# Kernel optimization log

Hardware: AMD Instinct MI355X
Metric: run time of the kernel (lower is better)

## Reference

```python
import jax, jax.numpy as jnp
import numpy as np

B, SEQ_IN, N, IN_DIM = 8, 12, 1000, 2
HID, HEADS = 128, 8
DH = HID // HEADS
E = 16000
INTERVAL, SCALE = 4, 1.0
LRELU_SLOPE = 0.2


def _layer_norm(x):
    # LayerNorm over last dim, elementwise_affine=False, eps=1e-5
    mu = jnp.mean(x, axis=-1, keepdims=True)
    var = jnp.mean((x - mu) ** 2, axis=-1, keepdims=True)
    return (x - mu) / jnp.sqrt(var + 1e-5)


def _edge_softmax(e, dst, n):
    # e: [E, HEADS]; softmax over edges sharing the same destination node
    m = jax.ops.segment_max(e, dst, num_segments=n)
    ex = jnp.exp(e - m[dst])
    s = jax.ops.segment_sum(ex, dst, num_segments=n)
    return ex / (s[dst] + 1e-16)


def _gat(x, src, dst, w_gat, a_l, a_r):
    # x: [B, N, HID] -> [B, N, HID]; single-layer multi-head GATConv
    b, n, _ = x.shape
    h = (x @ w_gat).reshape(b, n, HEADS, DH)
    el = jnp.einsum('bnhd,hd->bnh', h, a_l)
    er = jnp.einsum('bnhd,hd->bnh', h, a_r)
    e = jax.nn.leaky_relu(el[:, src] + er[:, dst], LRELU_SLOPE)  # [B, E, HEADS]
    alpha = jax.vmap(_edge_softmax, in_axes=(0, None, None))(e, dst, n)
    msg = h[:, src] * alpha[..., None]  # [B, E, HEADS, DH]
    agg = jax.vmap(lambda m: jax.ops.segment_sum(m, dst, num_segments=n))(msg)
    return agg.reshape(b, n, HID)


def _odeint_rk4(f, y0, t):
    # fixed-step RK4 over the time grid t (stand-in for torchdiffeq.odeint)
    def step(y, ts):
        t0, t1 = ts
        dt = t1 - t0
        k1 = f(y)
        k2 = f(y + 0.5 * dt * k1)
        k3 = f(y + 0.5 * dt * k2)
        k4 = f(y + dt * k3)
        return y + (dt / 6.0) * (k1 + 2.0 * k2 + 2.0 * k3 + k4), None
    y, _ = jax.lax.scan(jax.checkpoint(step), y0, (t[:-1], t[1:]))
    return y


def setup_inputs() -> dict:
    key = jax.random.key(0)
    ks = jax.random.split(key, 12)
    s = 0.05
    inputs = jax.random.normal(ks[0], (B, SEQ_IN, N, IN_DIM), dtype=jnp.float32)
    src = jax.random.randint(ks[1], (E,), 0, N, dtype=jnp.int32)
    dst = jax.random.randint(ks[2], (E,), 0, N, dtype=jnp.int32)
    w_in = jax.random.normal(ks[3], (IN_DIM, HID), jnp.float32) * s
    b_in = jnp.zeros((HID,), jnp.float32)
    w_gat = jax.random.normal(ks[4], (HID, HID), jnp.float32) * s
    a_l = jax.random.normal(ks[5], (HEADS, DH), jnp.float32) * s
    a_r = jax.random.normal(ks[6], (HEADS, DH), jnp.float32) * s
    w_W = jax.random.normal(ks[7], (HID, HID), jnp.float32) * s
    b_W = jnp.zeros((HID,), jnp.float32)
    w_U = jax.random.normal(ks[8], (HID, HID), jnp.float32) * s
    b_U = jnp.zeros((HID,), jnp.float32)
    w_o1 = jax.random.normal(ks[9], (HID, HID), jnp.float32) * s
    b_o1 = jnp.zeros((HID,), jnp.float32)
    w_o2 = jax.random.normal(ks[10], (HID, HID), jnp.float32) * s
    b_o2 = jnp.zeros((HID,), jnp.float32)
    return {"inputs": inputs, "src": src, "dst": dst, "w_in": w_in, "b_in": b_in,
            "w_gat": w_gat, "a_l": a_l, "a_r": a_r, "w_W": w_W, "b_W": b_W,
            "w_U": w_U, "b_U": b_U, "w_o1": w_o1, "b_o1": b_o1, "w_o2": w_o2, "b_o2": b_o2}


def reference(inputs, src, dst, w_in, b_in, w_gat, a_l, a_r, w_W, b_W,
              w_U, b_U, w_o1, b_o1, w_o2, b_o2):
    h = inputs @ w_in + b_in  # [B, SEQ_IN, N, HID]
    t = jnp.linspace(0.0, 1.0, INTERVAL + 1, dtype=jnp.float32) * SCALE
    f = lambda y: _gat(y, src, dst, w_gat, a_l, a_r)
    ret = h[:, 0]  # y0 = first timestep
    for idx in range(SEQ_IN):
        ret = _odeint_rk4(f, ret, t)  # take final time point
        if idx != 0:
            ret = jnp.tanh(ret @ w_W + b_W + h[:, idx] @ w_U + b_U)
        ret = _layer_norm(ret)
    out = ret[:, None]  # [B, 1, N, HID]  (view + unsqueeze + transpose)
    out = jnp.tanh(out @ w_o1 + b_o1) @ w_o2 + b_o2
    return out
```

## Files before the change

### kernel.cpp

```cpp
#include <hip/hip_runtime.h>

#define NNODE 1000
#define NBATCH 8
#define SEQL 12
#define NHEAD 8
#define DHEAD 16
#define HID 128
#define NEDGE 16000
#define NROWS (NBATCH*NNODE)
#define RPB 32
#define NBLK_P 256
#define NBLK_B 32
#define BARSTRIDE 64
#define PTHREADS 1024
#define ORPB 16
#define NBLK_O (NROWS/ORPB)
#define DT 0.25f
#define ECAP 768
#define SPIN_LIMIT 2000000ULL
#define WSTRIDE 136
#define WLO (128*WSTRIDE)
#define HSTR 144

#define OFF_MASK  32
#define OFF_GMASK 48
#define OFF_GCNT  56
#define HWREG_XCC_ID 6164


typedef unsigned short u16;
typedef unsigned int   u32;
typedef unsigned long long u64;
typedef __attribute__((ext_vector_type(8))) short bf16x8;
typedef __attribute__((ext_vector_type(4))) float f32x4;
typedef __attribute__((ext_vector_type(4))) unsigned int u32x4;

__device__ __forceinline__ u16 f2bf(float f){
  u32 x = __float_as_uint(f);
  return (u16)((x + 0x7fffu + ((x>>16)&1u)) >> 16);
}
__device__ __forceinline__ float bf2f(u16 u){ return __uint_as_float(((u32)u)<<16); }

__device__ __forceinline__ u64 ld_agent_u64(const u16* p){
  return __hip_atomic_load(reinterpret_cast<const u64*>(p),
                           __ATOMIC_RELAXED, __HIP_MEMORY_SCOPE_AGENT);
}
__device__ __forceinline__ void st_agent_u64(u16* p, u64 v){
  __hip_atomic_store(reinterpret_cast<u64*>(p), v,
                     __ATOMIC_RELAXED, __HIP_MEMORY_SCOPE_AGENT);
}
__device__ __forceinline__ float ld_agent_f32(const float* p){
  u32 v = __hip_atomic_load(reinterpret_cast<const u32*>(p),
                            __ATOMIC_RELAXED, __HIP_MEMORY_SCOPE_AGENT);
  return __uint_as_float(v);
}
__device__ __forceinline__ void st_agent_f32(float* p, float v){
  __hip_atomic_store(reinterpret_cast<u32*>(p), __float_as_uint(v),
                     __ATOMIC_RELAXED, __HIP_MEMORY_SCOPE_AGENT);
}

__device__ __forceinline__ void inv_l1(){
  asm volatile("buffer_inv sc0\n\ts_waitcnt vmcnt(0)" ::: "memory");
}

__device__ __forceinline__ int poll_l2(int* p){
  int exp = -1;
  __hip_atomic_compare_exchange_strong(p, &exp, -1,
      __ATOMIC_RELAXED, __ATOMIC_RELAXED, __HIP_MEMORY_SCOPE_WORKGROUP);
  return exp;
}

__device__ __forceinline__ void grid_bar2(int* bar, int target, bool l2){
  __syncthreads();
  if (threadIdx.x == 0){
    unsigned long long t0;
    if (l2){
      __hip_atomic_fetch_add(bar, 1, __ATOMIC_RELAXED, __HIP_MEMORY_SCOPE_WORKGROUP);
      t0 = __builtin_amdgcn_s_memrealtime();
      while (poll_l2(bar) < target){
        __builtin_amdgcn_s_sleep(2);
        if (__builtin_amdgcn_s_memrealtime() - t0 > SPIN_LIMIT) break;
      }
    } else {
      __hip_atomic_fetch_add(bar, 1, __ATOMIC_RELEASE, __HIP_MEMORY_SCOPE_AGENT);
      t0 = __builtin_amdgcn_s_memrealtime();
      while (__hip_atomic_load(bar, __ATOMIC_RELAXED, __HIP_MEMORY_SCOPE_AGENT) < target){
        __builtin_amdgcn_s_sleep(2);
        if (__builtin_amdgcn_s_memrealtime() - t0 > SPIN_LIMIT) break;
      }
    }
  }
  __syncthreads();
}

__device__ __forceinline__ void startup_bar(int* cnt){
  __syncthreads();
  if (threadIdx.x == 0){
    __hip_atomic_fetch_add(cnt, 1, __ATOMIC_RELEASE, __HIP_MEMORY_SCOPE_AGENT);
    unsigned long long t0 = __builtin_amdgcn_s_memrealtime();
    while (__hip_atomic_load(cnt, __ATOMIC_RELAXED, __HIP_MEMORY_SCOPE_AGENT) < NBLK_P){
      __builtin_amdgcn_s_sleep(2);
      if (__builtin_amdgcn_s_memrealtime() - t0 > SPIN_LIMIT) break;
    }
  }
  __syncthreads();
}

template<int NT>
__device__ __forceinline__ void load_W(float* Wl, const float* g, int tid){
  #pragma unroll
  for (int c = 0; c < (HID*HID/4)/NT; ++c){
    int e = (c*NT + tid)*4;
    *reinterpret_cast<float4*>(Wl + e) = *reinterpret_cast<const float4*>(g + e);
  }
}

__device__ __forceinline__ void load_WT_split(u16* WbT, const float* g, int tid){
  #pragma unroll
  for (int c = 0; c < 16; ++c){
    int flat = c*PTHREADS + tid;
    int k = flat >> 7, n = flat & 127;
    float v = g[flat];
    u16 hi = f2bf(v);
    u16 lo = f2bf(v - bf2f(hi));
    WbT[n*WSTRIDE + k]       = hi;
    WbT[WLO + n*WSTRIDE + k] = lo;
  }
}

__device__ __forceinline__ void gemm128_1(const float* Wl, const float* yt, int fg, int rs,
                                          float o[4]){
  float a0[4]={0.f,0.f,0.f,0.f};
  #pragma unroll 4
  for (int k=0;k<HID;k+=4){
    float4 ya = *reinterpret_cast<const float4*>(yt + rs*HID + k);
    #pragma unroll
    for (int kk=0;kk<4;++kk){
      const float* wr = Wl + (k+kk)*HID + fg*4;
      float av = (&ya.x)[kk];
      #pragma unroll
      for (int i=0;i<4;++i) a0[i] = fmaf(wr[i], av, a0[i]);
    }
  }
  #pragma unroll
  for (int i=0;i<4;++i) o[i]=a0[i];
}

template<int RSTEP>
__device__ __forceinline__ void gemm128(const float* Wl, const float* yt, int fg, int rs,
                                        float o0[4], float o1[4]){
  float a0[4]={0.f,0.f,0.f,0.f}, a1[4]={0.f,0.f,0.f,0.f};
  #pragma unroll 4
  for (int k=0;k<HID;k+=4){
    float4 ya = *reinterpret_cast<const float4*>(yt + rs*HID + k);
    float4 yb = *reinterpret_cast<const float4*>(yt + (rs+RSTEP)*HID + k);
    #pragma unroll
    for (int kk=0;kk<4;++kk){
      const float* wr = Wl + (k+kk)*HID + fg*4;
      float av = (&ya.x)[kk];
      float bv = (&yb.x)[kk];
      #pragma unroll
      for (int i=0;i<4;++i){
        float w = wr[i];
        a0[i] = fmaf(w, av, a0[i]);
        a1[i] = fmaf(w, bv, a1[i]);
      }
    }
  }
  #pragma unroll
  for (int i=0;i<4;++i){ o0[i]=a0[i]; o1[i]=a1[i]; }
}

__device__ __forceinline__ void pack_y(u16* yt_bf, int rA, int off8, const float y[8]){
  uint4 w;
  w.x = (u32)f2bf(y[0]) | ((u32)f2bf(y[1])<<16);
  w.y = (u32)f2bf(y[2]) | ((u32)f2bf(y[3])<<16);
  w.z = (u32)f2bf(y[4]) | ((u32)f2bf(y[5])<<16);
  w.w = (u32)f2bf(y[6]) | ((u32)f2bf(y[7])<<16);
  *reinterpret_cast<uint4*>(yt_bf + rA*WSTRIDE + off8) = w;
}

__device__ __forceinline__ void edge_acc(const u32x4 q, float el, float erh,
                                         float acc[8], float& sum){
  float hv[8];
  hv[0]=__uint_as_float(q[0]<<16); hv[1]=__uint_as_float(q[0]&0xffff0000u);
  hv[2]=__uint_as_float(q[1]<<16); hv[3]=__uint_as_float(q[1]&0xffff0000u);
  hv[4]=__uint_as_float(q[2]<<16); hv[5]=__uint_as_float(q[2]&0xffff0000u);
  hv[6]=__uint_as_float(q[3]<<16); hv[7]=__uint_as_float(q[3]&0xffff0000u);
  const float x = el + erh;
  const float w = __expf(fminf(fmaxf(x, 0.2f*x), 30.f));
  sum += w;
  #pragma unroll
  for (int i=0;i<8;++i) acc[i] = fmaf(w, hv[i], acc[i]);
}

template<bool L2>
__device__ __forceinline__ void gather_f(const u16* __restrict__ h_rd,
    const int* __restrict__ eptr, int e_lo, int e_hi, int sbase, int off8, int hd,
    float erh, float acc[8], float& sum)
{
  if constexpr (L2){
    int e = e_lo;
    for (; e + 4 <= e_hi; e += 4){
      const u16* r0 = h_rd + (size_t)(sbase + eptr[e+0])*HSTR;
      const u16* r1 = h_rd + (size_t)(sbase + eptr[e+1])*HSTR;
      const u16* r2 = h_rd + (size_t)(sbase + eptr[e+2])*HSTR;
      const u16* r3 = h_rd + (size_t)(sbase + eptr[e+3])*HSTR;
      u32x4 q0 = *reinterpret_cast<const u32x4*>(r0 + off8);
      u32x4 q1 = *reinterpret_cast<const u32x4*>(r1 + off8);
      u32x4 q2 = *reinterpret_cast<const u32x4*>(r2 + off8);
      u32x4 q3 = *reinterpret_cast<const u32x4*>(r3 + off8);
      float x0 = reinterpret_cast<const float*>(r0 + 128)[hd];
      float x1 = reinterpret_cast<const float*>(r1 + 128)[hd];
      float x2 = reinterpret_cast<const float*>(r2 + 128)[hd];
      float x3 = reinterpret_cast<const float*>(r3 + 128)[hd];
      edge_acc(q0, x0, erh, acc, sum);
      edge_acc(q1, x1, erh, acc, sum);
      edge_acc(q2, x2, erh, acc, sum);
      edge_acc(q3, x3, erh, acc, sum);
    }
    for (; e < e_hi; ++e){
      const u16* r = h_rd + (size_t)(sbase + eptr[e])*HSTR;
      u32x4 q = *reinterpret_cast<const u32x4*>(r + off8);
      float x = reinterpret_cast<const float*>(r + 128)[hd];
      edge_acc(q, x, erh, acc, sum);
    }
  } else {
    for (int e = e_lo; e < e_hi; ++e){
      const u16* r = h_rd + (size_t)(sbase + eptr[e])*HSTR;
      const u64 L = ld_agent_u64(r + off8);
      const u64 H = ld_agent_u64(r + off8 + 4);
      const float x = ld_agent_f32(reinterpret_cast<const float*>(r + 128) + hd);
      u32x4 v;
      v[0]=(u32)L; v[1]=(u32)(L>>32); v[2]=(u32)H; v[3]=(u32)(H>>32);
      edge_acc(v, x, erh, acc, sum);
    }
  }
}

__device__ __forceinline__ void h_stage(const u16* yt_bf, u16* ht_bf, const u16* WbT,
    int mt, int nt, int quad, int lc,
    int fg, int rs, int rowF, bool actF, bool l2,
    u16* __restrict__ h_wr, float* er_l, const float ar4[4], const float al4[4])
{
  f32x4 c0 = {0.f,0.f,0.f,0.f}, c1 = {0.f,0.f,0.f,0.f};
  const u16* arow = yt_bf + (mt*16 + lc)*WSTRIDE;
  const u16* brow = WbT  + (nt*16 + lc)*WSTRIDE;
  #pragma unroll
  for (int k0 = 0; k0 < 4; ++k0){
    const int off = k0*32 + quad*8;
    bf16x8 a  = *reinterpret_cast<const bf16x8*>(arow + off);
    bf16x8 bh = *reinterpret_cast<const bf16x8*>(brow + off);
    bf16x8 bl = *reinterpret_cast<const bf16x8*>(brow + WLO + off);
    if (k0 & 1){
      c1 = __builtin_amdgcn_mfma_f32_16x16x32_bf16(a, bh, c1, 0, 0, 0);
      c1 = __builtin_amdgcn_mfma_f32_16x16x32_bf16(a, bl, c1, 0, 0, 0);
    } else {
      c0 = __builtin_amdgcn_mfma_f32_16x16x32_bf16(a, bh, c0, 0, 0, 0);
      c0 = __builtin_amdgcn_mfma_f32_16x16x32_bf16(a, bl, c0, 0, 0, 0);
    }
  }
  {
    const int col = nt*16 + lc;
    #pragma unroll
    for (int r = 0; r < 4; ++r)
      ht_bf[(mt*16 + quad*4 + r)*WSTRIDE + col] = f2bf(c0[r] + c1[r]);
  }
  __syncthreads();
  const u64 pk = *reinterpret_cast<const u64*>(ht_bf + rs*WSTRIDE + fg*4);
  if (actF){
    if (l2) *reinterpret_cast<u64*>(h_wr + (size_t)rowF*HSTR + fg*4) = pk;
    else    st_agent_u64(h_wr + (size_t)rowF*HSTR + fg*4, pk);
  }
  const float h0 = bf2f((u16)pk),       h1 = bf2f((u16)(pk>>16));
  const float h2 = bf2f((u16)(pk>>32)), h3 = bf2f((u16)(pk>>48));
  float er = 0.f, el = 0.f;
  er = fmaf(h0, ar4[0], er); er = fmaf(h1, ar4[1], er);
  er = fmaf(h2, ar4[2], er); er = fmaf(h3, ar4[3], er);
  el = fmaf(h0, al4[0], el); el = fmaf(h1, al4[1], el);
  el = fmaf(h2, al4[2], el); el = fmaf(h3, al4[3], el);
  er += __shfl_xor(er,1); er += __shfl_xor(er,2);
  el += __shfl_xor(el,1); el += __shfl_xor(el,2);
  if ((fg & 3) == 0 && actF){
    er_l[rs*NHEAD + (fg>>2)] = er;
    float* elp = reinterpret_cast<float*>(h_wr + (size_t)rowF*HSTR + 128);
    if (l2) elp[fg>>2] = el;
    else    st_agent_f32(elp + (fg>>2), el);
  }
}

__global__ void csr_kernel(const int* __restrict__ src, const int* __restrict__ dst,
                           int* __restrict__ row_start, int* __restrict__ edge_src,
                           int* __restrict__ bar){
  __shared__ int cnt[1024];
  __shared__ int scanb[1024];
  __shared__ int cur[1024];
  int tid = threadIdx.x;
  if (tid < NBATCH*BARSTRIDE) bar[tid] = 0;
  cnt[tid] = 0;
  __syncthreads();
  for (int e = tid; e < NEDGE; e += 1024) atomicAdd(&cnt[dst[e]], 1);
  __syncthreads();
  int v = cnt[tid];
  scanb[tid] = v;
  __syncthreads();
  for (int off=1; off<1024; off<<=1){
    int t = (tid >= off) ? scanb[tid-off] : 0;
    __syncthreads();
    scanb[tid] += t;
    __syncthreads();
  }
  int incl = scanb[tid];
  if (tid < NNODE){ cur[tid] = incl - v; row_start[tid+1] = incl; }
  if (tid == 0) row_start[0] = 0;
  __syncthreads();
  for (int e = tid; e < NEDGE; e += 1024){
    int d = dst[e];
    int pos = atomicAdd(&cur[d], 1);
    edge_src[pos] = src[e];
  }
}

struct PArgs {
  u16* hb0; u16* hb1; float* y_out;
  const int* row_start; const int* edge_src;
  const float* w_gat; const float* a_l; const float* a_r;
  const float* inputs; const float* w_in; const float* b_in;
  const float* w_W; const float* b_W; const float* w_U; const float* b_U;
  int* bar;
};

__global__ void __launch_bounds__(PTHREADS, 4) persist(PArgs p)
{
  __shared__ __align__(16) u16 WbT[2*128*WSTRIDE];
  __shared__ __align__(16) u16 yt_bf[RPB*WSTRIDE];
  __shared__ __align__(16) u16 ht_bf[RPB*WSTRIDE];
  __shared__ float zt[RPB*HID];
  __shared__ int   esrc_l[ECAP];
  __shared__ int   eoff[RPB+1];
  __shared__ int   degs_s[RPB];
  __shared__ float er_l[RPB*NHEAD];
  __shared__ int   use_l2_s;
  float* const Wlf = reinterpret_cast<float*>(WbT);

  const int tid  = threadIdx.x;
  const int bat   = blockIdx.x & 7;
  const int slot  = blockIdx.x >> 3;
  const int row0  = bat * NNODE + slot * RPB;
  const int nrows = (slot == 31) ? (NNODE - 31*RPB) : RPB;
  int* const bar_b = p.bar + bat * BARSTRIDE;
  const int tA = tid & 15, seg = (tid >> 4) & 1, rA = tid >> 5;
  const bool actA = rA < nrows;
  const int nA     = slot*RPB + rA;
  const int nAs    = actA ? nA : 0;
  const int sbase  = bat * NNODE;
  const int hd   = tA >> 1;
  const int off8 = tA * 8;
  const int fg = tid & 31, rs = tid >> 5;
  const bool actF = rs < nrows;
  const int rowF = row0 + rs;
  const int hd2 = fg >> 2, db = (fg & 3) * 4;
  const int wv = tid >> 6, lane = tid & 63, quad = lane >> 4, lc = lane & 15;
  const int mt = wv & 1, nt = wv >> 1;

  int s0r = 0, degr = 0;
  if (actA){ s0r = p.row_start[nA]; degr = p.row_start[nA+1] - s0r; }
  if ((tid & 31) == 0) degs_s[rA] = degr;
  __syncthreads();
  if (tid == 0){
    int o = 0;
    #pragma unroll
    for (int r = 0; r < RPB; ++r){ eoff[r] = o; o += degs_s[r]; }
    eoff[RPB] = o;
  }
  __syncthreads();
  const int* eptr;
  if (eoff[RPB] <= ECAP){
    const int eb = eoff[rA];
    for (int e = tA + 16*seg; e < degr; e += 32) esrc_l[eb + e] = p.edge_src[s0r + e];
    eptr = esrc_l + eb;
  } else {
    eptr = p.edge_src + s0r;
  }

  float ar4[4], al4[4];
  #pragma unroll
  for (int i=0;i<4;++i){
    ar4[i] = p.a_r[hd2*DHEAD + db + i];
    al4[i] = p.a_l[hd2*DHEAD + db + i];
  }

  load_WT_split(WbT, p.w_gat, tid);

  float yb8[8], ya8[8];
  {
    const float x0 = p.inputs[((bat*SEQL + 0)*NNODE + nAs)*2 + 0];
    const float x1 = p.inputs[((bat*SEQL + 0)*NNODE + nAs)*2 + 1];
    #pragma unroll
    for (int i=0;i<8;++i){
      int f = off8 + i;
      yb8[i] = x0*p.w_in[f] + x1*p.w_in[HID+f] + p.b_in[f];
    }
    if (seg == 0) pack_y(yt_bf, rA, off8, yb8);
  }
  __syncthreads();
  h_stage(yt_bf, ht_bf, WbT, mt, nt, quad, lc, fg, rs, rowF, actF, false, p.hb0, er_l, ar4, al4);

  if (tid == 0){
    int xcc = (int)(__builtin_amdgcn_s_getreg(HWREG_XCC_ID) & 0xf);
    __hip_atomic_fetch_or(reinterpret_cast<u32*>(bar_b + OFF_MASK), 1u<<xcc,
                          __ATOMIC_RELAXED, __HIP_MEMORY_SCOPE_AGENT);
    __hip_atomic_fetch_or(reinterpret_cast<u32*>(p.bar + OFF_GMASK), 1u<<xcc,
                          __ATOMIC_RELAXED, __HIP_MEMORY_SCOPE_AGENT);
  }
  startup_bar(p.bar + OFF_GCNT);
  if (tid == 0){
    u32 mb = __hip_atomic_load(reinterpret_cast<u32*>(bar_b + OFF_MASK),
                               __ATOMIC_RELAXED, __HIP_MEMORY_SCOPE_AGENT);
    u32 mg = __hip_atomic_load(reinterpret_cast<u32*>(p.bar + OFF_GMASK),
                               __ATOMIC_RELAXED, __HIP_MEMORY_SCOPE_AGENT);
    use_l2_s = (__popc(mb) == 1 && __popc(mg) == 8) ? 1 : 0;
  }
  __syncthreads();
  const bool use_l2 = use_l2_s != 0;

  int step = 1;

  const int half0 = (degr + 1) >> 1;
  const int e_lo = seg ? half0 : 0;
  const int e_hi = seg ? degr  : half0;

  int rd = 0;
  for (int idx = 0; idx < SEQL; ++idx){
    for (int st = 0; st < 4; ++st){
      for (int j = 1; j <= 4; ++j){
        const u16* __restrict__ h_rd = rd ? p.hb1 : p.hb0;
        u16* __restrict__ h_wr       = rd ? p.hb0 : p.hb1;

        float acc[8] = {0.f,0.f,0.f,0.f,0.f,0.f,0.f,0.f};
        float sum = 0.f;
        {
          const float erh = er_l[rA*NHEAD + hd];
          if (use_l2){
            inv_l1();
            gather_f<true >(h_rd, eptr, e_lo, e_hi, sbase, off8, hd, erh, acc, sum);
          } else {
            gather_f<false>(h_rd, eptr, e_lo, e_hi, sbase, off8, hd, erh, acc, sum);
          }
        }
        sum += __shfl_xor(sum, 16);
        #pragma unroll
        for (int i=0;i<8;++i) acc[i] += __shfl_xor(acc[i], 16);
        const float inv = 1.f / (sum + 1e-16f);
        #pragma unroll
        for (int i=0;i<8;++i) acc[i] *= inv;

        const bool is5 = (st == 3) && (j == 4);
        float nxt[8];
        if (j == 1){
          #pragma unroll
          for (int i=0;i<8;++i){ ya8[i] = fmaf(DT/6.f, acc[i], yb8[i]);
                                 nxt[i] = fmaf(0.5f*DT, acc[i], yb8[i]); }
        } else if (j == 2){
          #pragma unroll
          for (int i=0;i<8;++i){ ya8[i] = fmaf(DT/3.f, acc[i], ya8[i]);
                                 nxt[i] = fmaf(0.5f*DT, acc[i], yb8[i]); }
        } else if (j == 3){
          #pragma unroll
          for (int i=0;i<8;++i){ ya8[i] = fmaf(DT/3.f, acc[i], ya8[i]);
                                 nxt[i] = fmaf(DT, acc[i], yb8[i]); }
        } else {
          #pragma unroll
          for (int i=0;i<8;++i) nxt[i] = fmaf(DT/6.f, acc[i], ya8[i]);
          if (!is5){
            #pragma unroll
            for (int i=0;i<8;++i) yb8[i] = nxt[i];
          }
        }

        if (!is5){
          if (seg == 0) pack_y(yt_bf, rA, off8, nxt);
          __syncthreads();
          h_stage(yt_bf, ht_bf, WbT, mt, nt, quad, lc, fg, rs, rowF, actF, use_l2, h_wr, er_l, ar4, al4);
          grid_bar2(bar_b, NBLK_B * step, use_l2); ++step;
          rd ^= 1;
          continue;
        }

        const bool last = (idx == SEQL-1);
        if (seg == 0){
          *reinterpret_cast<float4*>(zt + rA*HID + off8)     = make_float4(nxt[0],nxt[1],nxt[2],nxt[3]);
          *reinterpret_cast<float4*>(zt + rA*HID + off8 + 4) = make_float4(nxt[4],nxt[5],nxt[6],nxt[7]);
        }
        float z4[4];
        if (idx > 0){
          load_W<PTHREADS>(Wlf, p.w_W, tid);
          __syncthreads();
          gemm128_1(Wlf, zt, fg, rs, z4);
          __syncthreads();
          {
            const float x0 = p.inputs[((bat*SEQL + idx)*NNODE + nAs)*2 + 0];
            const float x1 = p.inputs[((bat*SEQL + idx)*NNODE + nAs)*2 + 1];
            if (seg == 0){
              float hv[8];
              #pragma unroll
              for (int i=0;i<8;++i){
                int f = off8 + i;
                hv[i] = x0*p.w_in[f] + x1*p.w_in[HID+f] + p.b_in[f];
              }
              *reinterpret_cast<float4*>(zt + rA*HID + off8)     = make_float4(hv[0],hv[1],hv[2],hv[3]);
              *reinterpret_cast<float4*>(zt + rA*HID + off8 + 4) = make_float4(hv[4],hv[5],hv[6],hv[7]);
            }
          }
          load_W<PTHREADS>(Wlf, p.w_U, tid);
          __syncthreads();
          float u4[4];
          gemm128_1(Wlf, zt, fg, rs, u4);
          #pragma unroll
          for (int i=0;i<4;++i)
            z4[i] = tanhf(z4[i] + u4[i] + p.b_W[fg*4+i] + p.b_U[fg*4+i]);
        } else {
          __syncthreads();
          #pragma unroll
          for (int i=0;i<4;++i) z4[i] = zt[rs*HID + fg*4 + i];
        }
        {
          float sv=0.f, qv=0.f;
          #pragma unroll
          for (int i=0;i<4;++i){ sv+=z4[i]; qv+=z4[i]*z4[i]; }
          #pragma unroll
          for (int off=1; off<32; off<<=1){
            sv += __shfl_xor(sv, off); qv += __shfl_xor(qv, off);
          }
          float mu = sv*(1.f/HID);
          float r  = rsqrtf(qv*(1.f/HID) - mu*mu + 1e-5f);
          #pragma unroll
          for (int i=0;i<4;++i) z4[i] = (z4[i]-mu)*r;
        }
        __syncthreads();
        *reinterpret_cast<float4*>(zt + rs*HID + fg*4) = make_float4(z4[0],z4[1],z4[2],z4[3]);
        if (last){
          if (actF)
            *reinterpret_cast<float4*>(p.y_out + (size_t)rowF*HID + fg*4) =
                make_float4(z4[0],z4[1],z4[2],z4[3]);
        } else {
          __syncthreads();
          if (idx > 0) load_WT_split(WbT, p.w_gat, tid);
          #pragma unroll
          for (int i=0;i<8;++i) yb8[i] = zt[rA*HID + off8 + i];
          if (seg == 0) pack_y(yt_bf, rA, off8, yb8);
          __syncthreads();
          h_stage(yt_bf, ht_bf, WbT, mt, nt, quad, lc, fg, rs, rowF, actF, use_l2, h_wr, er_l, ar4, al4);
          grid_bar2(bar_b, NBLK_B * step, use_l2); ++step;
          rd ^= 1;
        }
      }
    }
  }
}

__global__ void __launch_bounds__(256, 2) out_kernel(
    const float* __restrict__ y_base,
    const float* __restrict__ w_o1, const float* __restrict__ b_o1,
    const float* __restrict__ w_o2, const float* __restrict__ b_o2,
    float* __restrict__ out)
{
  __shared__ float Wl[HID*HID];
  __shared__ float yt[ORPB*HID];
  const int tid = threadIdx.x;
  const int row0 = blockIdx.x * ORPB;
  const int rA = tid >> 4, tA = tid & 15;
  const int rowA = row0 + rA;
  {
    float4 v0 = *reinterpret_cast<const float4*>(y_base + rowA*HID + tA*8);
    float4 v1 = *reinterpret_cast<const float4*>(y_base + rowA*HID + tA*8 + 4);
    *reinterpret_cast<float4*>(yt + rA*HID + tA*8)     = v0;
    *reinterpret_cast<float4*>(yt + rA*HID + tA*8 + 4) = v1;
  }
  load_W<256>(Wl, w_o1, tid);
  __syncthreads();
  const int fg = tid & 31, rs = tid >> 5;
  float t0[4], t1[4];
  gemm128<8>(Wl, yt, fg, rs, t0, t1);
  #pragma unroll
  for (int i=0;i<4;++i){
    float bb = b_o1[fg*4+i];
    t0[i] = tanhf(t0[i] + bb);
    t1[i] = tanhf(t1[i] + bb);
  }
  __syncthreads();
  *reinterpret_cast<float4*>(yt + rs*HID + fg*4)     = make_float4(t0[0],t0[1],t0[2],t0[3]);
  *reinterpret_cast<float4*>(yt + (rs+8)*HID + fg*4) = make_float4(t1[0],t1[1],t1[2],t1[3]);
  load_W<256>(Wl, w_o2, tid);
  __syncthreads();
  float o0[4], o1[4];
  gemm128<8>(Wl, yt, fg, rs, o0, o1);
  const int rowF0 = row0 + rs, rowF1 = row0 + rs + 8;
  *reinterpret_cast<float4*>(out + rowF0*HID + fg*4) =
      make_float4(o0[0]+b_o2[fg*4+0], o0[1]+b_o2[fg*4+1], o0[2]+b_o2[fg*4+2], o0[3]+b_o2[fg*4+3]);
  *reinterpret_cast<float4*>(out + rowF1*HID + fg*4) =
      make_float4(o1[0]+b_o2[fg*4+0], o1[1]+b_o2[fg*4+1], o1[2]+b_o2[fg*4+2], o1[3]+b_o2[fg*4+3]);
}

extern "C" void kernel_launch(void* const* d_in, const int* in_sizes, int n_in,
                              void* d_out, int out_size, void* d_ws, size_t ws_size,
                              hipStream_t stream)
{
  const float* inputs = (const float*)d_in[0];
  const int* src      = (const int*)d_in[1];
  const int* dst      = (const int*)d_in[2];
  const float* w_in   = (const float*)d_in[3];
  const float* b_in   = (const float*)d_in[4];
  const float* w_gat  = (const float*)d_in[5];
  const float* a_l    = (const float*)d_in[6];
  const float* a_r    = (const float*)d_in[7];
  const float* w_W    = (const float*)d_in[8];
  const float* b_W    = (const float*)d_in[9];
  const float* w_U    = (const float*)d_in[10];
  const float* b_U    = (const float*)d_in[11];
  const float* w_o1   = (const float*)d_in[12];
  const float* b_o1   = (const float*)d_in[13];
  const float* w_o2   = (const float*)d_in[14];
  const float* b_o2   = (const float*)d_in[15];

  const size_t RH  = (size_t)NROWS * HID;
  const size_t RH2 = (size_t)NROWS * HSTR;
  float* y_out = reinterpret_cast<float*>(d_ws);
  u16*   hbuf  = reinterpret_cast<u16*>(y_out + RH);
  u16*   hb0   = hbuf;
  u16*   hb1   = hbuf + RH2;
  int*   I     = reinterpret_cast<int*>(hbuf + 2*RH2);
  int* row_start = I;
  int* edge_src  = I + 1024;
  int* bar       = I + 1024 + NEDGE;

  size_t need = RH*sizeof(float) + 2*RH2*sizeof(u16)
              + (size_t)(1024 + NEDGE + NBATCH*BARSTRIDE)*sizeof(int);
  if (ws_size < need) return;

  csr_kernel<<<1, 1024, 0, stream>>>(src, dst, row_start, edge_src, bar);

  PArgs pa;
  pa.hb0 = hb0; pa.hb1 = hb1; pa.y_out = y_out;
  pa.row_start = row_start; pa.edge_src = edge_src;
  pa.w_gat = w_gat; pa.a_l = a_l; pa.a_r = a_r;
  pa.inputs = inputs; pa.w_in = w_in; pa.b_in = b_in;
  pa.w_W = w_W; pa.b_W = b_W; pa.w_U = w_U; pa.b_U = b_U;
  pa.bar = bar;

  persist<<<NBLK_P, PTHREADS, 0, stream>>>(pa);

  out_kernel<<<NBLK_O, 256, 0, stream>>>(y_out, w_o1, b_o1, w_o2, b_o2, (float*)d_out);
}
```

Measured before the change: 1.728 ms.

## Halve rows per block, switch GAT projection to fp16 MFMA, split edges four ways

Rows per persistent block drop from 32 to 16, which doubles the block count to 512 and raises the launch-bounds occupancy target to 8 blocks. The bf16 hi/lo split GEMM (two MFMAs per k step) becomes a single fp16 MFMA, and the weights and h storage move to fp16, roughly halving matrix-core work and the weight footprint in shared memory. Each destination row's edge gather is now split over four thread segments instead of two, with an extra shuffle reduction. The change trades precision (fp16 range and mantissa in place of the split bf16) and more grid-barrier participants per batch for extra parallelism.

```diff
diff --git a/kernel.cpp b/kernel.cpp
--- a/kernel.cpp
+++ b/kernel.cpp
@@ -8,9 +8,9 @@
 #define HID 128
 #define NEDGE 16000
 #define NROWS (NBATCH*NNODE)
-#define RPB 32
-#define NBLK_P 256
-#define NBLK_B 32
+#define RPB 16
+#define NBLK_P 512
+#define NBLK_B 64
 #define BARSTRIDE 64
 #define PTHREADS 1024
 #define ORPB 16
@@ -19,7 +19,6 @@
 #define ECAP 768
 #define SPIN_LIMIT 2000000ULL
 #define WSTRIDE 136
-#define WLO (128*WSTRIDE)
 #define HSTR 144
 
 #define OFF_MASK  32
@@ -31,15 +30,16 @@
 typedef unsigned short u16;
 typedef unsigned int   u32;
 typedef unsigned long long u64;
-typedef __attribute__((ext_vector_type(8))) short bf16x8;
+typedef __attribute__((ext_vector_type(8))) _Float16 f16x8;
 typedef __attribute__((ext_vector_type(4))) float f32x4;
 typedef __attribute__((ext_vector_type(4))) unsigned int u32x4;
 
-__device__ __forceinline__ u16 f2bf(float f){
-  u32 x = __float_as_uint(f);
-  return (u16)((x + 0x7fffu + ((x>>16)&1u)) >> 16);
-}
-__device__ __forceinline__ float bf2f(u16 u){ return __uint_as_float(((u32)u)<<16); }
+__device__ __forceinline__ u16 f2h(float f){
+  union { _Float16 h; u16 u; } cv; cv.h = (_Float16)f; return cv.u;
+}
+__device__ __forceinline__ float h2f(u16 u){
+  union { _Float16 h; u16 u; } cv; cv.u = u; return (float)cv.h;
+}
 
 __device__ __forceinline__ u64 ld_agent_u64(const u16* p){
   return __hip_atomic_load(reinterpret_cast<const u64*>(p),
@@ -115,31 +115,35 @@
   }
 }
 
-__device__ __forceinline__ void load_WT_split(u16* WbT, const float* g, int tid){
+__device__ __forceinline__ void load_W_f16(u16* Wg, const float* g, int tid){
+  #pragma unroll
+  for (int c = 0; c < (HID*HID)/PTHREADS; ++c){
+    int e = c*PTHREADS + tid;
+    Wg[e] = f2h(g[e]);
+  }
+}
+
+__device__ __forceinline__ void load_WT_f16(u16* Wb, const float* g, int tid){
   #pragma unroll
   for (int c = 0; c < 16; ++c){
     int flat = c*PTHREADS + tid;
     int k = flat >> 7, n = flat & 127;
-    float v = g[flat];
-    u16 hi = f2bf(v);
-    u16 lo = f2bf(v - bf2f(hi));
-    WbT[n*WSTRIDE + k]       = hi;
-    WbT[WLO + n*WSTRIDE + k] = lo;
-  }
-}
-
-__device__ __forceinline__ void gemm128_1(const float* Wl, const float* yt, int fg, int rs,
-                                          float o[4]){
+    Wb[n*WSTRIDE + k] = f2h(g[flat]);
+  }
+}
+
+__device__ __forceinline__ void gemm128_1h(const u16* Wg, const float* yt, int fg, int rs,
+                                           float o[4]){
   float a0[4]={0.f,0.f,0.f,0.f};
   #pragma unroll 4
   for (int k=0;k<HID;k+=4){
     float4 ya = *reinterpret_cast<const float4*>(yt + rs*HID + k);
     #pragma unroll
     for (int kk=0;kk<4;++kk){
-      const float* wr = Wl + (k+kk)*HID + fg*4;
+      const u16* wr = Wg + (k+kk)*HID + fg*4;
       float av = (&ya.x)[kk];
       #pragma unroll
-      for (int i=0;i<4;++i) a0[i] = fmaf(wr[i], av, a0[i]);
+      for (int i=0;i<4;++i) a0[i] = fmaf(h2f(wr[i]), av, a0[i]);
     }
   }
   #pragma unroll
@@ -171,22 +175,22 @@
   for (int i=0;i<4;++i){ o0[i]=a0[i]; o1[i]=a1[i]; }
 }
 
-__device__ __forceinline__ void pack_y(u16* yt_bf, int rA, int off8, const float y[8]){
+__device__ __forceinline__ void pack_y(u16* yt, int rA, int off8, const float y[8]){
   uint4 w;
-  w.x = (u32)f2bf(y[0]) | ((u32)f2bf(y[1])<<16);
-  w.y = (u32)f2bf(y[2]) | ((u32)f2bf(y[3])<<16);
-  w.z = (u32)f2bf(y[4]) | ((u32)f2bf(y[5])<<16);
-  w.w = (u32)f2bf(y[6]) | ((u32)f2bf(y[7])<<16);
-  *reinterpret_cast<uint4*>(yt_bf + rA*WSTRIDE + off8) = w;
+  w.x = (u32)f2h(y[0]) | ((u32)f2h(y[1])<<16);
+  w.y = (u32)f2h(y[2]) | ((u32)f2h(y[3])<<16);
+  w.z = (u32)f2h(y[4]) | ((u32)f2h(y[5])<<16);
+  w.w = (u32)f2h(y[6]) | ((u32)f2h(y[7])<<16);
+  *reinterpret_cast<uint4*>(yt + rA*WSTRIDE + off8) = w;
 }
 
 __device__ __forceinline__ void edge_acc(const u32x4 q, float el, float erh,
                                          float acc[8], float& sum){
   float hv[8];
-  hv[0]=__uint_as_float(q[0]<<16); hv[1]=__uint_as_float(q[0]&0xffff0000u);
-  hv[2]=__uint_as_float(q[1]<<16); hv[3]=__uint_as_float(q[1]&0xffff0000u);
-  hv[4]=__uint_as_float(q[2]<<16); hv[5]=__uint_as_float(q[2]&0xffff0000u);
-  hv[6]=__uint_as_float(q[3]<<16); hv[7]=__uint_as_float(q[3]&0xffff0000u);
+  hv[0]=h2f((u16)q[0]); hv[1]=h2f((u16)(q[0]>>16));
+  hv[2]=h2f((u16)q[1]); hv[3]=h2f((u16)(q[1]>>16));
+  hv[4]=h2f((u16)q[2]); hv[5]=h2f((u16)(q[2]>>16));
+  hv[6]=h2f((u16)q[3]); hv[7]=h2f((u16)(q[3]>>16));
   const float x = el + erh;
   const float w = __expf(fminf(fmaxf(x, 0.2f*x), 30.f));
   sum += w;
@@ -238,42 +242,36 @@
   }
 }
 
-__device__ __forceinline__ void h_stage(const u16* yt_bf, u16* ht_bf, const u16* WbT,
-    int mt, int nt, int quad, int lc,
-    int fg, int rs, int rowF, bool actF, bool l2,
+__device__ __forceinline__ void h_stage(const u16* yt, u16* ht, const u16* Wb,
+    int wv, int quad, int lc,
+    int fg, int rs, int rsF, int rowF, bool actF, bool l2,
     u16* __restrict__ h_wr, float* er_l, const float ar4[4], const float al4[4])
 {
-  f32x4 c0 = {0.f,0.f,0.f,0.f}, c1 = {0.f,0.f,0.f,0.f};
-  const u16* arow = yt_bf + (mt*16 + lc)*WSTRIDE;
-  const u16* brow = WbT  + (nt*16 + lc)*WSTRIDE;
-  #pragma unroll
-  for (int k0 = 0; k0 < 4; ++k0){
-    const int off = k0*32 + quad*8;
-    bf16x8 a  = *reinterpret_cast<const bf16x8*>(arow + off);
-    bf16x8 bh = *reinterpret_cast<const bf16x8*>(brow + off);
-    bf16x8 bl = *reinterpret_cast<const bf16x8*>(brow + WLO + off);
-    if (k0 & 1){
-      c1 = __builtin_amdgcn_mfma_f32_16x16x32_bf16(a, bh, c1, 0, 0, 0);
-      c1 = __builtin_amdgcn_mfma_f32_16x16x32_bf16(a, bl, c1, 0, 0, 0);
-    } else {
-      c0 = __builtin_amdgcn_mfma_f32_16x16x32_bf16(a, bh, c0, 0, 0, 0);
-      c0 = __builtin_amdgcn_mfma_f32_16x16x32_bf16(a, bl, c0, 0, 0, 0);
-    }
-  }
-  {
-    const int col = nt*16 + lc;
+  if (wv < 8){
+    f32x4 c0 = {0.f,0.f,0.f,0.f}, c1 = {0.f,0.f,0.f,0.f};
+    const u16* arow = yt + lc*WSTRIDE;
+    const u16* brow = Wb + (wv*16 + lc)*WSTRIDE;
+    #pragma unroll
+    for (int k0 = 0; k0 < 4; ++k0){
+      const int off = k0*32 + quad*8;
+      f16x8 a = *reinterpret_cast<const f16x8*>(arow + off);
+      f16x8 b = *reinterpret_cast<const f16x8*>(brow + off);
+      if (k0 & 1) c1 = __builtin_amdgcn_mfma_f32_16x16x32_f16(a, b, c1, 0, 0, 0);
+      else        c0 = __builtin_amdgcn_mfma_f32_16x16x32_f16(a, b, c0, 0, 0, 0);
+    }
+    const int col = wv*16 + lc;
     #pragma unroll
     for (int r = 0; r < 4; ++r)
-      ht_bf[(mt*16 + quad*4 + r)*WSTRIDE + col] = f2bf(c0[r] + c1[r]);
-  }
-  __syncthreads();
-  const u64 pk = *reinterpret_cast<const u64*>(ht_bf + rs*WSTRIDE + fg*4);
+      ht[(quad*4 + r)*WSTRIDE + col] = f2h(c0[r] + c1[r]);
+  }
+  __syncthreads();
+  const u64 pk = *reinterpret_cast<const u64*>(ht + rsF*WSTRIDE + fg*4);
   if (actF){
     if (l2) *reinterpret_cast<u64*>(h_wr + (size_t)rowF*HSTR + fg*4) = pk;
     else    st_agent_u64(h_wr + (size_t)rowF*HSTR + fg*4, pk);
   }
-  const float h0 = bf2f((u16)pk),       h1 = bf2f((u16)(pk>>16));
-  const float h2 = bf2f((u16)(pk>>32)), h3 = bf2f((u16)(pk>>48));
+  const float h0 = h2f((u16)pk),       h1 = h2f((u16)(pk>>16));
+  const float h2 = h2f((u16)(pk>>32)), h3 = h2f((u16)(pk>>48));
   float er = 0.f, el = 0.f;
   er = fmaf(h0, ar4[0], er); er = fmaf(h1, ar4[1], er);
   er = fmaf(h2, ar4[2], er); er = fmaf(h3, ar4[3], er);
@@ -282,7 +280,7 @@
   er += __shfl_xor(er,1); er += __shfl_xor(er,2);
   el += __shfl_xor(el,1); el += __shfl_xor(el,2);
   if ((fg & 3) == 0 && actF){
-    er_l[rs*NHEAD + (fg>>2)] = er;
+    er_l[rsF*NHEAD + (fg>>2)] = er;
     float* elp = reinterpret_cast<float*>(h_wr + (size_t)rowF*HSTR + 128);
     if (l2) elp[fg>>2] = el;
     else    st_agent_f32(elp + (fg>>2), el);
@@ -330,9 +328,9 @@
   int* bar;
 };
 
-__global__ void __launch_bounds__(PTHREADS, 4) persist(PArgs p)
+__global__ void __launch_bounds__(PTHREADS, 8) persist(PArgs p)
 {
-  __shared__ __align__(16) u16 WbT[2*128*WSTRIDE];
+  __shared__ __align__(16) u16 WbT[128*WSTRIDE];
   __shared__ __align__(16) u16 yt_bf[RPB*WSTRIDE];
   __shared__ __align__(16) u16 ht_bf[RPB*WSTRIDE];
   __shared__ float zt[RPB*HID];
@@ -341,31 +339,31 @@
   __shared__ int   degs_s[RPB];
   __shared__ float er_l[RPB*NHEAD];
   __shared__ int   use_l2_s;
-  float* const Wlf = reinterpret_cast<float*>(WbT);
+  u16* const Wg = WbT;
 
   const int tid  = threadIdx.x;
   const int bat   = blockIdx.x & 7;
   const int slot  = blockIdx.x >> 3;
   const int row0  = bat * NNODE + slot * RPB;
-  const int nrows = (slot == 31) ? (NNODE - 31*RPB) : RPB;
+  int nr = NNODE - slot*RPB;
+  const int nrows = nr < 0 ? 0 : (nr > RPB ? RPB : nr);
   int* const bar_b = p.bar + bat * BARSTRIDE;
-  const int tA = tid & 15, seg = (tid >> 4) & 1, rA = tid >> 5;
+  const int tA = tid & 15, seg = (tid >> 4) & 3, rA = tid >> 6;
   const bool actA = rA < nrows;
   const int nA     = slot*RPB + rA;
   const int nAs    = actA ? nA : 0;
   const int sbase  = bat * NNODE;
   const int hd   = tA >> 1;
   const int off8 = tA * 8;
-  const int fg = tid & 31, rs = tid >> 5;
+  const int fg = tid & 31, rs = tid >> 5, rsF = rs & (RPB-1);
   const bool actF = rs < nrows;
   const int rowF = row0 + rs;
   const int hd2 = fg >> 2, db = (fg & 3) * 4;
   const int wv = tid >> 6, lane = tid & 63, quad = lane >> 4, lc = lane & 15;
-  const int mt = wv & 1, nt = wv >> 1;
 
   int s0r = 0, degr = 0;
   if (actA){ s0r = p.row_start[nA]; degr = p.row_start[nA+1] - s0r; }
-  if ((tid & 31) == 0) degs_s[rA] = degr;
+  if ((tid & 63) == 0) degs_s[rA] = degr;
   __syncthreads();
   if (tid == 0){
     int o = 0;
@@ -377,7 +375,7 @@
   const int* eptr;
   if (eoff[RPB] <= ECAP){
     const int eb = eoff[rA];
-    for (int e = tA + 16*seg; e < degr; e += 32) esrc_l[eb + e] = p.edge_src[s0r + e];
+    for (int e = tA + 16*seg; e < degr; e += 64) esrc_l[eb + e] = p.edge_src[s0r + e];
     eptr = esrc_l + eb;
   } else {
     eptr = p.edge_src + s0r;
@@ -390,7 +388,7 @@
     al4[i] = p.a_l[hd2*DHEAD + db + i];
   }
 
-  load_WT_split(WbT, p.w_gat, tid);
+  load_WT_f16(WbT, p.w_gat, tid);
 
   float yb8[8], ya8[8];
   {
@@ -404,7 +402,8 @@
     if (seg == 0) pack_y(yt_bf, rA, off8, yb8);
   }
   __syncthreads();
-  h_stage(yt_bf, ht_bf, WbT, mt, nt, quad, lc, fg, rs, rowF, actF, false, p.hb0, er_l, ar4, al4);
+  h_stage(yt_bf, ht_bf, WbT, wv, quad, lc, fg, rs, rsF, rowF, actF, false,
+          p.hb0, er_l, ar4, al4);
 
   if (tid == 0){
     int xcc = (int)(__builtin_amdgcn_s_getreg(HWREG_XCC_ID) & 0xf);
@@ -426,9 +425,8 @@
 
   int step = 1;
 
-  const int half0 = (degr + 1) >> 1;
-  const int e_lo = seg ? half0 : 0;
-  const int e_hi = seg ? degr  : half0;
+  const int e_lo = (seg * degr) >> 2;
+  const int e_hi = ((seg + 1) * degr) >> 2;
 
   int rd = 0;
   for (int idx = 0; idx < SEQL; ++idx){
@@ -449,8 +447,12 @@
           }
         }
         sum += __shfl_xor(sum, 16);
+        sum += __shfl_xor(sum, 32);
         #pragma unroll
-        for (int i=0;i<8;++i) acc[i] += __shfl_xor(acc[i], 16);
+        for (int i=0;i<8;++i){
+          acc[i] += __shfl_xor(acc[i], 16);
+          acc[i] += __shfl_xor(acc[i], 32);
+        }
         const float inv = 1.f / (sum + 1e-16f);
         #pragma unroll
         for (int i=0;i<8;++i) acc[i] *= inv;
@@ -481,7 +483,8 @@
         if (!is5){
           if (seg == 0) pack_y(yt_bf, rA, off8, nxt);
           __syncthreads();
-          h_stage(yt_bf, ht_bf, WbT, mt, nt, quad, lc, fg, rs, rowF, actF, use_l2, h_wr, er_l, ar4, al4);
+          h_stage(yt_bf, ht_bf, WbT, wv, quad, lc, fg, rs, rsF, rowF, actF, use_l2,
+                  h_wr, er_l, ar4, al4);
           grid_bar2(bar_b, NBLK_B * step, use_l2); ++step;
           rd ^= 1;
           continue;
@@ -494,9 +497,9 @@
         }
         float z4[4];
         if (idx > 0){
-          load_W<PTHREADS>(Wlf, p.w_W, tid);
+          load_W_f16(Wg, p.w_W, tid);
           __syncthreads();
-          gemm128_1(Wlf, zt, fg, rs, z4);
+          gemm128_1h(Wg, zt, fg, rsF, z4);
           __syncthreads();
           {
             const float x0 = p.inputs[((bat*SEQL + idx)*NNODE + nAs)*2 + 0];
@@ -512,17 +515,17 @@
               *reinterpret_cast<float4*>(zt + rA*HID + off8 + 4) = make_float4(hv[4],hv[5],hv[6],hv[7]);
             }
           }
-          load_W<PTHREADS>(Wlf, p.w_U, tid);
+          load_W_f16(Wg, p.w_U, tid);
           __syncthreads();
           float u4[4];
-          gemm128_1(Wlf, zt, fg, rs, u4);
+          gemm128_1h(Wg, zt, fg, rsF, u4);
           #pragma unroll
           for (int i=0;i<4;++i)
             z4[i] = tanhf(z4[i] + u4[i] + p.b_W[fg*4+i] + p.b_U[fg*4+i]);
         } else {
           __syncthreads();
           #pragma unroll
-          for (int i=0;i<4;++i) z4[i] = zt[rs*HID + fg*4 + i];
+          for (int i=0;i<4;++i) z4[i] = zt[rsF*HID + fg*4 + i];
         }
         {
           float sv=0.f, qv=0.f;
@@ -538,19 +541,21 @@
           for (int i=0;i<4;++i) z4[i] = (z4[i]-mu)*r;
         }
         __syncthreads();
-        *reinterpret_cast<float4*>(zt + rs*HID + fg*4) = make_float4(z4[0],z4[1],z4[2],z4[3]);
+        if (rs < RPB)
+          *reinterpret_cast<float4*>(zt + rs*HID + fg*4) = make_float4(z4[0],z4[1],z4[2],z4[3]);
         if (last){
           if (actF)
             *reinterpret_cast<float4*>(p.y_out + (size_t)rowF*HID + fg*4) =
                 make_float4(z4[0],z4[1],z4[2],z4[3]);
         } else {
           __syncthreads();
-          if (idx > 0) load_WT_split(WbT, p.w_gat, tid);
+          if (idx > 0) load_WT_f16(WbT, p.w_gat, tid);
           #pragma unroll
           for (int i=0;i<8;++i) yb8[i] = zt[rA*HID + off8 + i];
           if (seg == 0) pack_y(yt_bf, rA, off8, yb8);
           __syncthreads();
-          h_stage(yt_bf, ht_bf, WbT, mt, nt, quad, lc, fg, rs, rowF, actF, use_l2, h_wr, er_l, ar4, al4);
+          h_stage(yt_bf, ht_bf, WbT, wv, quad, lc, fg, rs, rsF, rowF, actF, use_l2,
+                  h_wr, er_l, ar4, al4);
           grid_bar2(bar_b, NBLK_B * step, use_l2); ++step;
           rd ^= 1;
         }
```

New measurement: 6.101 ms. 253% more time.
